# Kernel optimization log

Measured on AMD Instinct MI355X. Metric: run time of the kernel, lower is better.

## Reference

```python
import jax, jax.numpy as jnp
import numpy as np

B, N, D_IN, D_OUT = 16, 4096, 256, 128


def setup_inputs() -> dict:
    key = jax.random.key(0)
    ks = jax.random.split(key, 7)
    s_proj = float(np.sqrt(2.0 / D_IN))   # kaiming-ish scale
    s_mlp = float(np.sqrt(2.0 / D_OUT))
    return {
        "X": jax.random.normal(ks[0], (B, N, D_IN), dtype=jnp.float32),
        "W_proj": jax.random.normal(ks[1], (D_IN, D_OUT), dtype=jnp.float32) * s_proj,
        "b_proj": jnp.zeros((D_OUT,), dtype=jnp.float32),
        "W1": jax.random.normal(ks[2], (D_OUT, D_OUT), dtype=jnp.float32) * s_mlp,
        "b1": jnp.zeros((D_OUT,), dtype=jnp.float32),
        "W2": jax.random.normal(ks[3], (D_OUT, D_OUT), dtype=jnp.float32) * s_mlp,
        "b2": jnp.zeros((D_OUT,), dtype=jnp.float32),
    }


def reference(X, W_proj, b_proj, W1, b1, W2, b2):
    # proj: Linear(input_dim, output_dim)
    X = jnp.einsum("bnd,de->bne", X, W_proj) + b_proj
    # mlp: FeedForwardNetwork(D,D,D, num_layers=2) == Linear -> ReLU -> Linear
    X = jax.nn.relu(jnp.einsum("bnd,de->bne", X, W1) + b1)
    X = jnp.einsum("bnd,de->bne", X, W2) + b2
    # leave-one-out sum over the N axis: for each row i, sum of all rows j != i.
    # Identical math to the masked (B,N,N,D) expand-reduce in the torch source.
    return X.sum(axis=1, keepdims=True) - X
```

## Files before the change

### kernel.cpp

```cpp
#include <hip/hip_runtime.h>
#include <stdint.h>

#define D_IN  256
#define D_OUT 128
#define NSEQ  4096
#define NB    16
#define TILE_M 64
#define GRID_M ((NB * NSEQ) / TILE_M)
#define LDS_BYTES 32768

typedef __bf16 bf16x8 __attribute__((ext_vector_type(8)));
typedef float  f32x4  __attribute__((ext_vector_type(4)));

__device__ __forceinline__ unsigned short f2bf(float f) {
  __bf16 h = (__bf16)f;
  union { __bf16 h; unsigned short u; } c; c.h = h;
  return c.u;
}
__device__ __forceinline__ float bf2f(unsigned short u) {
  union { unsigned int u; float f; } a; a.u = ((unsigned int)u) << 16;
  return a.f;
}

__global__ __launch_bounds__(256) void prep_weights(
    const float* __restrict__ Wp, const float* __restrict__ W1, const float* __restrict__ W2,
    unsigned short* __restrict__ WpT, unsigned short* __restrict__ W1T, unsigned short* __restrict__ W2T) {
  int t = blockIdx.x * 256 + threadIdx.x;
  if (t < 256 * 128) {
    int k = t >> 7, n = t & 127;
    WpT[n * 256 + k] = f2bf(Wp[t]);
  } else if (t < 256 * 128 + 128 * 128) {
    int t2 = t - 256 * 128; int k = t2 >> 7, n = t2 & 127;
    W1T[n * 128 + k] = f2bf(W1[t2]);
  } else {
    int t3 = t - 256 * 128 - 128 * 128; int k = t3 >> 7, n = t3 & 127;
    W2T[n * 128 + k] = f2bf(W2[t3]);
  }
}

template <bool USE_WS>
__global__ __launch_bounds__(256, 2) void fused3(
    const float* __restrict__ X,
    const unsigned short* __restrict__ WpT,
    const unsigned short* __restrict__ W1T,
    const unsigned short* __restrict__ W2T,
    const float* __restrict__ bproj, const float* __restrict__ b1v, const float* __restrict__ b2v,
    unsigned short* __restrict__ Y3, float* __restrict__ out, float* __restrict__ P) {
  extern __shared__ unsigned short smem[];
  unsigned short* bufA = smem;
  unsigned short* bufB = smem + 8192;

  const int tid  = threadIdx.x;
  const int lane = tid & 63;
  const int w    = tid >> 6;
  const int q    = lane >> 4;
  const int l16  = lane & 15;
  const int rowbase = blockIdx.x * TILE_M;
  const int col0 = w * 32 + l16;
  const int col1 = col0 + 16;

  bf16x8 wp0[2][4], wp1[2][4], w1f[2][4], w2f[2][4];
#pragma unroll
  for (int ks = 0; ks < 4; ++ks) {
    wp0[0][ks] = *(const bf16x8*)(WpT + (size_t)col0 * 256 + ks * 32 + q * 8);
    wp0[1][ks] = *(const bf16x8*)(WpT + (size_t)col1 * 256 + ks * 32 + q * 8);
    wp1[0][ks] = *(const bf16x8*)(WpT + (size_t)col0 * 256 + 128 + ks * 32 + q * 8);
    wp1[1][ks] = *(const bf16x8*)(WpT + (size_t)col1 * 256 + 128 + ks * 32 + q * 8);
    w1f[0][ks] = *(const bf16x8*)(W1T + (size_t)col0 * 128 + ks * 32 + q * 8);
    w1f[1][ks] = *(const bf16x8*)(W1T + (size_t)col1 * 128 + ks * 32 + q * 8);
    w2f[0][ks] = *(const bf16x8*)(W2T + (size_t)col0 * 128 + ks * 32 + q * 8);
    w2f[1][ks] = *(const bf16x8*)(W2T + (size_t)col1 * 128 + ks * 32 + q * 8);
  }
  __builtin_amdgcn_sched_barrier(0);

#pragma unroll
  for (int it = 0; it < 8; ++it) {
    int i = tid + it * 256;
    int r = i >> 5, c4 = (i & 31) << 2;
    const float4 v = *(const float4*)(X + (size_t)(rowbase + r) * D_IN + c4);
    ushort4 u; u.x = f2bf(v.x); u.y = f2bf(v.y); u.z = f2bf(v.z); u.w = f2bf(v.w);
    *(ushort4*)(bufA + r * 128 + ((((c4 >> 3) ^ (r & 15)) << 3) + (c4 & 7))) = u;
  }

  f32x4 acc[4][2];
#pragma unroll
  for (int rt = 0; rt < 4; ++rt) {
    acc[rt][0] = (f32x4){0.f, 0.f, 0.f, 0.f};
    acc[rt][1] = (f32x4){0.f, 0.f, 0.f, 0.f};
  }
  __syncthreads();

  float4 xv[8];
#pragma unroll
  for (int it = 0; it < 8; ++it) {
    int i = tid + it * 256;
    int r = i >> 5, c4 = (i & 31) << 2;
    xv[it] = *(const float4*)(X + (size_t)(rowbase + r) * D_IN + 128 + c4);
  }

#pragma unroll
  for (int ks = 0; ks < 4; ++ks)
#pragma unroll
    for (int rt = 0; rt < 4; ++rt) {
      bf16x8 a = *(const bf16x8*)(bufA + (rt * 16 + l16) * 128 + (((4 * ks + q) ^ l16) << 3));
      acc[rt][0] = __builtin_amdgcn_mfma_f32_16x16x32_bf16(a, wp0[0][ks], acc[rt][0], 0, 0, 0);
      acc[rt][1] = __builtin_amdgcn_mfma_f32_16x16x32_bf16(a, wp0[1][ks], acc[rt][1], 0, 0, 0);
    }

#pragma unroll
  for (int it = 0; it < 8; ++it) {
    int i = tid + it * 256;
    int r = i >> 5, c4 = (i & 31) << 2;
    ushort4 u; u.x = f2bf(xv[it].x); u.y = f2bf(xv[it].y); u.z = f2bf(xv[it].z); u.w = f2bf(xv[it].w);
    *(ushort4*)(bufB + r * 128 + ((((c4 >> 3) ^ (r & 15)) << 3) + (c4 & 7))) = u;
  }
  __syncthreads();

#pragma unroll
  for (int ks = 0; ks < 4; ++ks)
#pragma unroll
    for (int rt = 0; rt < 4; ++rt) {
      bf16x8 a = *(const bf16x8*)(bufB + (rt * 16 + l16) * 128 + (((4 * ks + q) ^ l16) << 3));
      acc[rt][0] = __builtin_amdgcn_mfma_f32_16x16x32_bf16(a, wp1[0][ks], acc[rt][0], 0, 0, 0);
      acc[rt][1] = __builtin_amdgcn_mfma_f32_16x16x32_bf16(a, wp1[1][ks], acc[rt][1], 0, 0, 0);
    }

  {
    const float bp0 = bproj[col0], bp1 = bproj[col1];
#pragma unroll
    for (int rt = 0; rt < 4; ++rt)
#pragma unroll
      for (int r = 0; r < 4; ++r) {
        int row = rt * 16 + q * 4 + r;
        int sw = (row & 15) << 3;
        bufA[row * 128 + ((((col0 >> 3) << 3) ^ sw) + (col0 & 7))] = f2bf(acc[rt][0][r] + bp0);
        bufA[row * 128 + ((((col1 >> 3) << 3) ^ sw) + (col1 & 7))] = f2bf(acc[rt][1][r] + bp1);
      }
  }
  __syncthreads();

#pragma unroll
  for (int rt = 0; rt < 4; ++rt) {
    acc[rt][0] = (f32x4){0.f, 0.f, 0.f, 0.f};
    acc[rt][1] = (f32x4){0.f, 0.f, 0.f, 0.f};
  }
#pragma unroll
  for (int ks = 0; ks < 4; ++ks)
#pragma unroll
    for (int rt = 0; rt < 4; ++rt) {
      bf16x8 a = *(const bf16x8*)(bufA + (rt * 16 + l16) * 128 + (((4 * ks + q) ^ l16) << 3));
      acc[rt][0] = __builtin_amdgcn_mfma_f32_16x16x32_bf16(a, w1f[0][ks], acc[rt][0], 0, 0, 0);
      acc[rt][1] = __builtin_amdgcn_mfma_f32_16x16x32_bf16(a, w1f[1][ks], acc[rt][1], 0, 0, 0);
    }

  {
    const float bb0 = b1v[col0], bb1 = b1v[col1];
#pragma unroll
    for (int rt = 0; rt < 4; ++rt)
#pragma unroll
      for (int r = 0; r < 4; ++r) {
        int row = rt * 16 + q * 4 + r;
        int sw = (row & 15) << 3;
        float v0 = acc[rt][0][r] + bb0; v0 = v0 > 0.f ? v0 : 0.f;
        float v1 = acc[rt][1][r] + bb1; v1 = v1 > 0.f ? v1 : 0.f;
        bufB[row * 128 + ((((col0 >> 3) << 3) ^ sw) + (col0 & 7))] = f2bf(v0);
        bufB[row * 128 + ((((col1 >> 3) << 3) ^ sw) + (col1 & 7))] = f2bf(v1);
      }
  }
  __syncthreads();

#pragma unroll
  for (int rt = 0; rt < 4; ++rt) {
    acc[rt][0] = (f32x4){0.f, 0.f, 0.f, 0.f};
    acc[rt][1] = (f32x4){0.f, 0.f, 0.f, 0.f};
  }
#pragma unroll
  for (int ks = 0; ks < 4; ++ks)
#pragma unroll
    for (int rt = 0; rt < 4; ++rt) {
      bf16x8 a = *(const bf16x8*)(bufB + (rt * 16 + l16) * 128 + (((4 * ks + q) ^ l16) << 3));
      acc[rt][0] = __builtin_amdgcn_mfma_f32_16x16x32_bf16(a, w2f[0][ks], acc[rt][0], 0, 0, 0);
      acc[rt][1] = __builtin_amdgcn_mfma_f32_16x16x32_bf16(a, w2f[1][ks], acc[rt][1], 0, 0, 0);
    }

  {
    const float bb0 = b2v[col0], bb1 = b2v[col1];
    float s0 = 0.f, s1 = 0.f;
#pragma unroll
    for (int rt = 0; rt < 4; ++rt)
#pragma unroll
      for (int r = 0; r < 4; ++r) {
        int row = rt * 16 + q * 4 + r;
        int sw = (row & 15) << 3;
        float v0 = acc[rt][0][r] + bb0;
        float v1 = acc[rt][1][r] + bb1;
        s0 += v0; s1 += v1;
        bufA[row * 128 + ((((col0 >> 3) << 3) ^ sw) + (col0 & 7))] = f2bf(v0);
        bufA[row * 128 + ((((col1 >> 3) << 3) ^ sw) + (col1 & 7))] = f2bf(v1);
      }
    s0 += __shfl_down(s0, 16); s0 += __shfl_down(s0, 32);
    s1 += __shfl_down(s1, 16); s1 += __shfl_down(s1, 32);
    if (lane < 16) {
      P[(size_t)blockIdx.x * 128 + col0] = s0;
      P[(size_t)blockIdx.x * 128 + col1] = s1;
    }
  }
  __syncthreads();

  if (USE_WS) {
#pragma unroll
    for (int it = 0; it < 4; ++it) {
      int i = tid + it * 256;
      int r = i >> 4, g = i & 15;
      *(uint4*)(Y3 + (size_t)(rowbase + r) * 128 + g * 8) =
          *(const uint4*)(bufA + r * 128 + ((g ^ (r & 15)) << 3));
    }
  } else {
#pragma unroll
    for (int it = 0; it < 8; ++it) {
      int i = tid + it * 256;
      int r = i >> 5, c4 = (i & 31) << 2;
      ushort4 u = *(const ushort4*)(bufA + r * 128 + ((((c4 >> 3) ^ (r & 15)) << 3) + (c4 & 7)));
      float4 v; v.x = bf2f(u.x); v.y = bf2f(u.y); v.z = bf2f(u.z); v.w = bf2f(u.w);
      *(float4*)(out + (size_t)(rowbase + r) * D_OUT + c4) = v;
    }
  }
}

__global__ __launch_bounds__(256) void reduce_S(const float* __restrict__ P, float* __restrict__ S) {
  __shared__ float tmp[128];
  int b = blockIdx.x;
  int col = threadIdx.x & 127;
  int h = threadIdx.x >> 7;
  float s = 0.f;
#pragma unroll
  for (int i = 0; i < 32; ++i) s += P[(size_t)(b * 64 + h * 32 + i) * 128 + col];
  if (h == 1) tmp[col] = s;
  __syncthreads();
  if (h == 0) S[b * 128 + col] = s + tmp[col];
}

__global__ __launch_bounds__(256) void finalize_ws(
    float* __restrict__ out, const unsigned short* __restrict__ Y3, const float* __restrict__ S) {
  size_t g = (size_t)blockIdx.x * 256 + threadIdx.x;
  size_t base = g * 8;
  int row = (int)(base >> 7);
  int col = (int)(base & 127);
  int b = row >> 12;
  uint4 u = *(const uint4*)(Y3 + base);
  float4 s0 = *(const float4*)(S + (b << 7) + col);
  float4 s1 = *(const float4*)(S + (b << 7) + col + 4);
  union { unsigned int uu; float f; } t;
  float4 o0, o1;
  t.uu = u.x << 16;          o0.x = s0.x - t.f;
  t.uu = u.x & 0xFFFF0000u;  o0.y = s0.y - t.f;
  t.uu = u.y << 16;          o0.z = s0.z - t.f;
  t.uu = u.y & 0xFFFF0000u;  o0.w = s0.w - t.f;
  t.uu = u.z << 16;          o1.x = s1.x - t.f;
  t.uu = u.z & 0xFFFF0000u;  o1.y = s1.y - t.f;
  t.uu = u.w << 16;          o1.z = s1.z - t.f;
  t.uu = u.w & 0xFFFF0000u;  o1.w = s1.w - t.f;
  *(float4*)(out + base) = o0;
  *(float4*)(out + base + 4) = o1;
}

__global__ __launch_bounds__(256) void finalize_ip(float* __restrict__ out, const float* __restrict__ S) {
  size_t g = (size_t)blockIdx.x * 256 + threadIdx.x;
  size_t base = g * 8;
  int row = (int)(base >> 7);
  int col = (int)(base & 127);
  int b = row >> 12;
  float4 s0 = *(const float4*)(S + (b << 7) + col);
  float4 s1 = *(const float4*)(S + (b << 7) + col + 4);
  float4 y0 = *(const float4*)(out + base);
  float4 y1 = *(const float4*)(out + base + 4);
  float4 o0, o1;
  o0.x = s0.x - y0.x; o0.y = s0.y - y0.y; o0.z = s0.z - y0.z; o0.w = s0.w - y0.w;
  o1.x = s1.x - y1.x; o1.y = s1.y - y1.y; o1.z = s1.z - y1.z; o1.w = s1.w - y1.w;
  *(float4*)(out + base) = o0;
  *(float4*)(out + base + 4) = o1;
}

extern "C" void kernel_launch(void* const* d_in, const int* in_sizes, int n_in,
                              void* d_out, int out_size, void* d_ws, size_t ws_size,
                              hipStream_t stream) {
  const float* X  = (const float*)d_in[0];
  const float* Wp = (const float*)d_in[1];
  const float* bp = (const float*)d_in[2];
  const float* W1 = (const float*)d_in[3];
  const float* b1 = (const float*)d_in[4];
  const float* W2 = (const float*)d_in[5];
  const float* b2 = (const float*)d_in[6];
  float* out = (float*)d_out;

  char* ws = (char*)d_ws;
  float* S = (float*)ws;
  unsigned short* WpT = (unsigned short*)(ws + 8192);
  unsigned short* W1T = (unsigned short*)(ws + 8192 + 65536);
  unsigned short* W2T = (unsigned short*)(ws + 8192 + 65536 + 32768);
  float* P = (float*)(ws + 8192 + 131072);
  unsigned short* Y3 = (unsigned short*)(ws + 8192 + 131072 + 524288);

  const size_t need = 8192 + 131072 + 524288 + (size_t)NB * NSEQ * D_OUT * 2;
  const bool use_ws = ws_size >= need;

  prep_weights<<<256, 256, 0, stream>>>(Wp, W1, W2, WpT, W1T, W2T);

  const int fin_blocks = (NB * NSEQ * D_OUT) / (8 * 256);
  if (use_ws) {
    fused3<true><<<GRID_M, 256, LDS_BYTES, stream>>>(X, WpT, W1T, W2T, bp, b1, b2, Y3, out, P);
    reduce_S<<<NB, 256, 0, stream>>>(P, S);
    finalize_ws<<<fin_blocks, 256, 0, stream>>>(out, Y3, S);
  } else {
    fused3<false><<<GRID_M, 256, LDS_BYTES, stream>>>(X, WpT, W1T, W2T, bp, b1, b2, Y3, out, P);
    reduce_S<<<NB, 256, 0, stream>>>(P, S);
    finalize_ip<<<fin_blocks, 256, 0, stream>>>(out, S);
  }
}
```

Baseline: 137.2 us.

## Fold projection and first MLP linear into one precomputed weight matrix

Since there is no nonlinearity between the projection and the first MLP linear, the prep kernel now computes Wp·W1 and the combined bias bp·W1+b1 on device. The main kernel then does two GEMMs per tile instead of three. This saves a third of the MFMA work and one LDS round trip, and it frees registers so occupancy can rise to 3 blocks per CU. The cost is a slightly different bf16 rounding path, plus a small fp32 matmul in the prep kernel that runs on every call.

```diff
diff --git a/kernel.cpp b/kernel.cpp
--- a/kernel.cpp
+++ b/kernel.cpp
@@ -22,29 +22,42 @@
   return a.f;
 }
 
-__global__ __launch_bounds__(256) void prep_weights(
+__global__ __launch_bounds__(256) void prep(
     const float* __restrict__ Wp, const float* __restrict__ W1, const float* __restrict__ W2,
-    unsigned short* __restrict__ WpT, unsigned short* __restrict__ W1T, unsigned short* __restrict__ W2T) {
-  int t = blockIdx.x * 256 + threadIdx.x;
-  if (t < 256 * 128) {
+    const float* __restrict__ bp, const float* __restrict__ b1,
+    unsigned short* __restrict__ WaT, unsigned short* __restrict__ W2T, float* __restrict__ be1) {
+  int b = blockIdx.x;
+  if (b < 128) {
+    __shared__ float wp[256];
+    int k0 = b * 2;
+    wp[threadIdx.x] = Wp[k0 * 128 + threadIdx.x];
+    __syncthreads();
+    int kk = threadIdx.x >> 7, n = threadIdx.x & 127;
+    float s = 0.f;
+#pragma unroll 16
+    for (int j = 0; j < 128; ++j) s += wp[kk * 128 + j] * W1[j * 128 + n];
+    WaT[n * 256 + (k0 + kk)] = f2bf(s);
+  } else if (b < 192) {
+    int t = (b - 128) * 256 + threadIdx.x;
     int k = t >> 7, n = t & 127;
-    WpT[n * 256 + k] = f2bf(Wp[t]);
-  } else if (t < 256 * 128 + 128 * 128) {
-    int t2 = t - 256 * 128; int k = t2 >> 7, n = t2 & 127;
-    W1T[n * 128 + k] = f2bf(W1[t2]);
+    W2T[n * 128 + k] = f2bf(W2[t]);
   } else {
-    int t3 = t - 256 * 128 - 128 * 128; int k = t3 >> 7, n = t3 & 127;
-    W2T[n * 128 + k] = f2bf(W2[t3]);
+    if (threadIdx.x < 128) {
+      int n = threadIdx.x;
+      float s = b1[n];
+#pragma unroll 16
+      for (int j = 0; j < 128; ++j) s += bp[j] * W1[j * 128 + n];
+      be1[n] = s;
+    }
   }
 }
 
 template <bool USE_WS>
-__global__ __launch_bounds__(256, 2) void fused3(
+__global__ __launch_bounds__(256, 3) void fused2(
     const float* __restrict__ X,
-    const unsigned short* __restrict__ WpT,
-    const unsigned short* __restrict__ W1T,
+    const unsigned short* __restrict__ WaT,
     const unsigned short* __restrict__ W2T,
-    const float* __restrict__ bproj, const float* __restrict__ b1v, const float* __restrict__ b2v,
+    const float* __restrict__ be1, const float* __restrict__ b2v,
     unsigned short* __restrict__ Y3, float* __restrict__ out, float* __restrict__ P) {
   extern __shared__ unsigned short smem[];
   unsigned short* bufA = smem;
@@ -59,19 +72,14 @@
   const int col0 = w * 32 + l16;
   const int col1 = col0 + 16;
 
-  bf16x8 wp0[2][4], wp1[2][4], w1f[2][4], w2f[2][4];
+  f32x4 acc[4][2];
+  bf16x8 bA[4][2], bB[4][2];
+
 #pragma unroll
   for (int ks = 0; ks < 4; ++ks) {
-    wp0[0][ks] = *(const bf16x8*)(WpT + (size_t)col0 * 256 + ks * 32 + q * 8);
-    wp0[1][ks] = *(const bf16x8*)(WpT + (size_t)col1 * 256 + ks * 32 + q * 8);
-    wp1[0][ks] = *(const bf16x8*)(WpT + (size_t)col0 * 256 + 128 + ks * 32 + q * 8);
-    wp1[1][ks] = *(const bf16x8*)(WpT + (size_t)col1 * 256 + 128 + ks * 32 + q * 8);
-    w1f[0][ks] = *(const bf16x8*)(W1T + (size_t)col0 * 128 + ks * 32 + q * 8);
-    w1f[1][ks] = *(const bf16x8*)(W1T + (size_t)col1 * 128 + ks * 32 + q * 8);
-    w2f[0][ks] = *(const bf16x8*)(W2T + (size_t)col0 * 128 + ks * 32 + q * 8);
-    w2f[1][ks] = *(const bf16x8*)(W2T + (size_t)col1 * 128 + ks * 32 + q * 8);
-  }
-  __builtin_amdgcn_sched_barrier(0);
+    bA[ks][0] = *(const bf16x8*)(WaT + (size_t)col0 * 256 + ks * 32 + q * 8);
+    bA[ks][1] = *(const bf16x8*)(WaT + (size_t)col1 * 256 + ks * 32 + q * 8);
+  }
 
 #pragma unroll
   for (int it = 0; it < 8; ++it) {
@@ -82,7 +90,6 @@
     *(ushort4*)(bufA + r * 128 + ((((c4 >> 3) ^ (r & 15)) << 3) + (c4 & 7))) = u;
   }
 
-  f32x4 acc[4][2];
 #pragma unroll
   for (int rt = 0; rt < 4; ++rt) {
     acc[rt][0] = (f32x4){0.f, 0.f, 0.f, 0.f};
@@ -97,14 +104,19 @@
     int r = i >> 5, c4 = (i & 31) << 2;
     xv[it] = *(const float4*)(X + (size_t)(rowbase + r) * D_IN + 128 + c4);
   }
+#pragma unroll
+  for (int ks = 0; ks < 4; ++ks) {
+    bB[ks][0] = *(const bf16x8*)(WaT + (size_t)col0 * 256 + 128 + ks * 32 + q * 8);
+    bB[ks][1] = *(const bf16x8*)(WaT + (size_t)col1 * 256 + 128 + ks * 32 + q * 8);
+  }
 
 #pragma unroll
   for (int ks = 0; ks < 4; ++ks)
 #pragma unroll
     for (int rt = 0; rt < 4; ++rt) {
       bf16x8 a = *(const bf16x8*)(bufA + (rt * 16 + l16) * 128 + (((4 * ks + q) ^ l16) << 3));
-      acc[rt][0] = __builtin_amdgcn_mfma_f32_16x16x32_bf16(a, wp0[0][ks], acc[rt][0], 0, 0, 0);
-      acc[rt][1] = __builtin_amdgcn_mfma_f32_16x16x32_bf16(a, wp0[1][ks], acc[rt][1], 0, 0, 0);
+      acc[rt][0] = __builtin_amdgcn_mfma_f32_16x16x32_bf16(a, bA[ks][0], acc[rt][0], 0, 0, 0);
+      acc[rt][1] = __builtin_amdgcn_mfma_f32_16x16x32_bf16(a, bA[ks][1], acc[rt][1], 0, 0, 0);
     }
 
 #pragma unroll
@@ -117,24 +129,32 @@
   __syncthreads();
 
 #pragma unroll
+  for (int ks = 0; ks < 4; ++ks) {
+    bA[ks][0] = *(const bf16x8*)(W2T + (size_t)col0 * 128 + ks * 32 + q * 8);
+    bA[ks][1] = *(const bf16x8*)(W2T + (size_t)col1 * 128 + ks * 32 + q * 8);
+  }
+
+#pragma unroll
   for (int ks = 0; ks < 4; ++ks)
 #pragma unroll
     for (int rt = 0; rt < 4; ++rt) {
       bf16x8 a = *(const bf16x8*)(bufB + (rt * 16 + l16) * 128 + (((4 * ks + q) ^ l16) << 3));
-      acc[rt][0] = __builtin_amdgcn_mfma_f32_16x16x32_bf16(a, wp1[0][ks], acc[rt][0], 0, 0, 0);
-      acc[rt][1] = __builtin_amdgcn_mfma_f32_16x16x32_bf16(a, wp1[1][ks], acc[rt][1], 0, 0, 0);
+      acc[rt][0] = __builtin_amdgcn_mfma_f32_16x16x32_bf16(a, bB[ks][0], acc[rt][0], 0, 0, 0);
+      acc[rt][1] = __builtin_amdgcn_mfma_f32_16x16x32_bf16(a, bB[ks][1], acc[rt][1], 0, 0, 0);
     }
 
   {
-    const float bp0 = bproj[col0], bp1 = bproj[col1];
+    const float e0 = be1[col0], e1 = be1[col1];
 #pragma unroll
     for (int rt = 0; rt < 4; ++rt)
 #pragma unroll
       for (int r = 0; r < 4; ++r) {
         int row = rt * 16 + q * 4 + r;
         int sw = (row & 15) << 3;
-        bufA[row * 128 + ((((col0 >> 3) << 3) ^ sw) + (col0 & 7))] = f2bf(acc[rt][0][r] + bp0);
-        bufA[row * 128 + ((((col1 >> 3) << 3) ^ sw) + (col1 & 7))] = f2bf(acc[rt][1][r] + bp1);
+        float v0 = acc[rt][0][r] + e0; v0 = v0 > 0.f ? v0 : 0.f;
+        float v1 = acc[rt][1][r] + e1; v1 = v1 > 0.f ? v1 : 0.f;
+        bufA[row * 128 + ((((col0 >> 3) << 3) ^ sw) + (col0 & 7))] = f2bf(v0);
+        bufA[row * 128 + ((((col1 >> 3) << 3) ^ sw) + (col1 & 7))] = f2bf(v1);
       }
   }
   __syncthreads();
@@ -149,38 +169,8 @@
 #pragma unroll
     for (int rt = 0; rt < 4; ++rt) {
       bf16x8 a = *(const bf16x8*)(bufA + (rt * 16 + l16) * 128 + (((4 * ks + q) ^ l16) << 3));
-      acc[rt][0] = __builtin_amdgcn_mfma_f32_16x16x32_bf16(a, w1f[0][ks], acc[rt][0], 0, 0, 0);
-      acc[rt][1] = __builtin_amdgcn_mfma_f32_16x16x32_bf16(a, w1f[1][ks], acc[rt][1], 0, 0, 0);
-    }
-
-  {
-    const float bb0 = b1v[col0], bb1 = b1v[col1];
-#pragma unroll
-    for (int rt = 0; rt < 4; ++rt)
-#pragma unroll
-      for (int r = 0; r < 4; ++r) {
-        int row = rt * 16 + q * 4 + r;
-        int sw = (row & 15) << 3;
-        float v0 = acc[rt][0][r] + bb0; v0 = v0 > 0.f ? v0 : 0.f;
-        float v1 = acc[rt][1][r] + bb1; v1 = v1 > 0.f ? v1 : 0.f;
-        bufB[row * 128 + ((((col0 >> 3) << 3) ^ sw) + (col0 & 7))] = f2bf(v0);
-        bufB[row * 128 + ((((col1 >> 3) << 3) ^ sw) + (col1 & 7))] = f2bf(v1);
-      }
-  }
-  __syncthreads();
-
-#pragma unroll
-  for (int rt = 0; rt < 4; ++rt) {
-    acc[rt][0] = (f32x4){0.f, 0.f, 0.f, 0.f};
-    acc[rt][1] = (f32x4){0.f, 0.f, 0.f, 0.f};
-  }
-#pragma unroll
-  for (int ks = 0; ks < 4; ++ks)
-#pragma unroll
-    for (int rt = 0; rt < 4; ++rt) {
-      bf16x8 a = *(const bf16x8*)(bufB + (rt * 16 + l16) * 128 + (((4 * ks + q) ^ l16) << 3));
-      acc[rt][0] = __builtin_amdgcn_mfma_f32_16x16x32_bf16(a, w2f[0][ks], acc[rt][0], 0, 0, 0);
-      acc[rt][1] = __builtin_amdgcn_mfma_f32_16x16x32_bf16(a, w2f[1][ks], acc[rt][1], 0, 0, 0);
+      acc[rt][0] = __builtin_amdgcn_mfma_f32_16x16x32_bf16(a, bA[ks][0], acc[rt][0], 0, 0, 0);
+      acc[rt][1] = __builtin_amdgcn_mfma_f32_16x16x32_bf16(a, bA[ks][1], acc[rt][1], 0, 0, 0);
     }
 
   {
@@ -195,8 +185,8 @@
         float v0 = acc[rt][0][r] + bb0;
         float v1 = acc[rt][1][r] + bb1;
         s0 += v0; s1 += v1;
-        bufA[row * 128 + ((((col0 >> 3) << 3) ^ sw) + (col0 & 7))] = f2bf(v0);
-        bufA[row * 128 + ((((col1 >> 3) << 3) ^ sw) + (col1 & 7))] = f2bf(v1);
+        bufB[row * 128 + ((((col0 >> 3) << 3) ^ sw) + (col0 & 7))] = f2bf(v0);
+        bufB[row * 128 + ((((col1 >> 3) << 3) ^ sw) + (col1 & 7))] = f2bf(v1);
       }
     s0 += __shfl_down(s0, 16); s0 += __shfl_down(s0, 32);
     s1 += __shfl_down(s1, 16); s1 += __shfl_down(s1, 32);
@@ -213,14 +203,14 @@
       int i = tid + it * 256;
       int r = i >> 4, g = i & 15;
       *(uint4*)(Y3 + (size_t)(rowbase + r) * 128 + g * 8) =
-          *(const uint4*)(bufA + r * 128 + ((g ^ (r & 15)) << 3));
+          *(const uint4*)(bufB + r * 128 + ((g ^ (r & 15)) << 3));
     }
   } else {
 #pragma unroll
     for (int it = 0; it < 8; ++it) {
       int i = tid + it * 256;
       int r = i >> 5, c4 = (i & 31) << 2;
-      ushort4 u = *(const ushort4*)(bufA + r * 128 + ((((c4 >> 3) ^ (r & 15)) << 3) + (c4 & 7)));
+      ushort4 u = *(const ushort4*)(bufB + r * 128 + ((((c4 >> 3) ^ (r & 15)) << 3) + (c4 & 7)));
       float4 v; v.x = bf2f(u.x); v.y = bf2f(u.y); v.z = bf2f(u.z); v.w = bf2f(u.w);
       *(float4*)(out + (size_t)(rowbase + r) * D_OUT + c4) = v;
     }
@@ -294,25 +284,25 @@
   float* out = (float*)d_out;
 
   char* ws = (char*)d_ws;
-  float* S = (float*)ws;
-  unsigned short* WpT = (unsigned short*)(ws + 8192);
-  unsigned short* W1T = (unsigned short*)(ws + 8192 + 65536);
-  unsigned short* W2T = (unsigned short*)(ws + 8192 + 65536 + 32768);
-  float* P = (float*)(ws + 8192 + 131072);
-  unsigned short* Y3 = (unsigned short*)(ws + 8192 + 131072 + 524288);
-
-  const size_t need = 8192 + 131072 + 524288 + (size_t)NB * NSEQ * D_OUT * 2;
+  float* S            = (float*)ws;
+  float* be1          = (float*)(ws + 8192);
+  unsigned short* WaT = (unsigned short*)(ws + 12288);
+  unsigned short* W2T = (unsigned short*)(ws + 12288 + 65536);
+  float* P            = (float*)(ws + 12288 + 65536 + 32768);
+  unsigned short* Y3  = (unsigned short*)(ws + 12288 + 65536 + 32768 + 524288);
+
+  const size_t need = 12288 + 65536 + 32768 + 524288 + (size_t)NB * NSEQ * D_OUT * 2;
   const bool use_ws = ws_size >= need;
 
-  prep_weights<<<256, 256, 0, stream>>>(Wp, W1, W2, WpT, W1T, W2T);
+  prep<<<193, 256, 0, stream>>>(Wp, W1, W2, bp, b1, WaT, W2T, be1);
 
   const int fin_blocks = (NB * NSEQ * D_OUT) / (8 * 256);
   if (use_ws) {
-    fused3<true><<<GRID_M, 256, LDS_BYTES, stream>>>(X, WpT, W1T, W2T, bp, b1, b2, Y3, out, P);
+    fused2<true><<<GRID_M, 256, LDS_BYTES, stream>>>(X, WaT, W2T, be1, b2, Y3, out, P);
     reduce_S<<<NB, 256, 0, stream>>>(P, S);
     finalize_ws<<<fin_blocks, 256, 0, stream>>>(out, Y3, S);
   } else {
-    fused3<false><<<GRID_M, 256, LDS_BYTES, stream>>>(X, WpT, W1T, W2T, bp, b1, b2, Y3, out, P);
+    fused2<false><<<GRID_M, 256, LDS_BYTES, stream>>>(X, WaT, W2T, be1, b2, Y3, out, P);
     reduce_S<<<NB, 256, 0, stream>>>(P, S);
     finalize_ip<<<fin_blocks, 256, 0, stream>>>(out, S);
   }
```

Measured after the change: 134.0 us. 1.02x faster.
